# Kernel optimization log

Measured on AMD Instinct MI355X. Metric: run time of the kernel, lower is better.

## Reference

```python
import jax, jax.numpy as jnp
import numpy as np

B, S, H, U = 32, 2048, 1024, 1024


def setup_inputs() -> dict:
    key = jax.random.key(0)
    ks = jax.random.split(key, 8)
    sH = 1.0 / np.sqrt(H)
    sU = 1.0 / np.sqrt(U)
    return {
        "encoder_output": jax.random.normal(ks[0], (B, S, H), dtype=jnp.float32),
        "last_layer_h_n": jax.random.normal(ks[1], (B, H), dtype=jnp.float32),
        # torch Linear stores weight [out,in]; we store transposed [in,out] for x @ W
        "W1_w": jax.random.uniform(ks[2], (H, U), jnp.float32, -sH, sH),
        "W1_b": jax.random.uniform(ks[3], (U,), jnp.float32, -sH, sH),
        "W2_w": jax.random.uniform(ks[4], (H, U), jnp.float32, -sH, sH),
        "W2_b": jax.random.uniform(ks[5], (U,), jnp.float32, -sH, sH),
        "V_w": jax.random.uniform(ks[6], (U, 1), jnp.float32, -sU, sU),
        "V_b": jax.random.uniform(ks[7], (1,), jnp.float32, -sU, sU),
    }


def reference(encoder_output, last_layer_h_n, W1_w, W1_b, W2_w, W2_b, V_w, V_b):
    # proj_enc: [B,S,U]; proj_h: [B,1,U] (unsqueeze(1) broadcast)
    proj_enc = jnp.einsum("bsh,hu->bsu", encoder_output, W1_w) + W1_b
    proj_h = (last_layer_h_n @ W2_w + W2_b)[:, None, :]
    # score: [B,S,1]
    score = jnp.tanh(proj_enc + proj_h) @ V_w + V_b
    # softmax over the sequence axis (dim 1)
    attention_weights = jax.nn.softmax(score, axis=1)
    # NOTE: in the original module context_vector is always None (dead branch),
    # so the faithful output is attention_weights alone.
    return attention_weights
```

## Files before the change

### kernel.cpp

```cpp
#include <hip/hip_runtime.h>
#include <hip/hip_bf16.h>


typedef __bf16 bf16x8 __attribute__((ext_vector_type(8)));
typedef float  f32x4  __attribute__((ext_vector_type(4)));

#define HDIM 1024
#define UDIM 1024
#define SDIM 2048
#define MROWS 65536
#define BM 128
#define BN 128
#define BK 32

__device__ inline unsigned short f2bf(float x) {
    return __builtin_bit_cast(unsigned short, (__bf16)x);
}

__device__ inline float fast_tanh(float x) {
    float z = __expf(-2.0f * __builtin_fabsf(x));
    float t = __fdividef(1.0f - z, 1.0f + z);
    return __builtin_copysignf(t, x);
}

#define GLDS16(gp, lp)                                                              \
    __builtin_amdgcn_global_load_lds(                                               \
        (const __attribute__((address_space(1))) unsigned int*)(gp),                \
        (__attribute__((address_space(3))) unsigned int*)(lp), 16, 0, 0)

__global__ __launch_bounds__(256) void cvt_kernel(const float* __restrict__ in,
                                                  unsigned short* __restrict__ out) {
    size_t i = ((size_t)blockIdx.x * 256 + threadIdx.x) * 8;
    const float4 f0 = *(const float4*)(in + i);
    const float4 f1 = *(const float4*)(in + i + 4);
    ushort4 h0, h1;
    h0.x = f2bf(f0.x); h0.y = f2bf(f0.y); h0.z = f2bf(f0.z); h0.w = f2bf(f0.w);
    h1.x = f2bf(f1.x); h1.y = f2bf(f1.y); h1.z = f2bf(f1.z); h1.w = f2bf(f1.w);
    *(ushort4*)(out + i) = h0;
    *(ushort4*)(out + i + 4) = h1;
}

__global__ void w1t_kernel(const float* __restrict__ W1, unsigned short* __restrict__ W1T) {
    __shared__ float tile[32][33];
    int bx = blockIdx.x;
    int by = blockIdx.y;
    int tx = threadIdx.x, ty = threadIdx.y;
#pragma unroll
    for (int r = 0; r < 4; ++r) {
        int h = by * 32 + ty + r * 8;
        int u = bx * 32 + tx;
        tile[ty + r * 8][tx] = W1[h * UDIM + u];
    }
    __syncthreads();
#pragma unroll
    for (int r = 0; r < 4; ++r) {
        int u = bx * 32 + ty + r * 8;
        int h = by * 32 + tx;
        W1T[u * HDIM + h] = f2bf(tile[tx][ty + r * 8]);
    }
}

__global__ void php_kernel(const float* __restrict__ hn, const float* __restrict__ W2,
                           float* __restrict__ php) {
    int u = (blockIdx.x & 3) * 256 + threadIdx.x;
    int b = blockIdx.y;
    int hc = blockIdx.z;
    int h0 = hc * 128;
    float acc = 0.f;
#pragma unroll 8
    for (int h = h0; h < h0 + 128; ++h)
        acc = fmaf(hn[b * HDIM + h], W2[h * UDIM + u], acc);
    php[(hc * 32 + b) * UDIM + u] = acc;
}

__global__ void ph_combine(const float* __restrict__ php, const float* __restrict__ W1b,
                           const float* __restrict__ W2b, float* __restrict__ ph) {
    int idx = blockIdx.x * 256 + threadIdx.x;
    int u = idx & (UDIM - 1);
    int b = idx >> 10;
    float acc = W1b[u] + W2b[u];
#pragma unroll
    for (int p = 0; p < 8; ++p) acc += php[(p * 32 + b) * UDIM + u];
    ph[idx] = acc;
}

__global__ __launch_bounds__(256) void score_kernel(
    const unsigned short* __restrict__ encb, const unsigned short* __restrict__ W1T,
    const float* __restrict__ ph, const float* __restrict__ Vw,
    float* __restrict__ part) {
    __shared__ unsigned short As[BM * BK];
    __shared__ unsigned short Bs[BN * BK];

    const int bx = blockIdx.x;
    const int x = bx & 7;
    const int k = bx >> 3;
    const int tile_n = k & 7;
    const int tile_m = (x << 6) | (k >> 3);

    const int t = threadIdx.x;
    const int lane = t & 63;
    const int wid = t >> 6;
    const int wm = wid >> 1, wn = wid & 1;

    const int row0 = tile_m * BM;
    const int col0 = tile_n * BN;

    f32x4 acc[4][4];
#pragma unroll
    for (int i = 0; i < 4; ++i)
#pragma unroll
        for (int j = 0; j < 4; ++j)
            acc[i][j] = (f32x4){0.f, 0.f, 0.f, 0.f};

    const int mrow = lane & 15;
    const int kcs = ((lane >> 4) ^ ((mrow >> 1) & 3)) * 8;

    const int c0 = wid * 64 + lane;
    const int c1 = c0 + 256;
    const int r0c = c0 >> 2, r1c = c1 >> 2;
    const int kl0 = ((c0 & 3) ^ ((c0 >> 3) & 3)) * 8;
    const int kl1 = ((c1 & 3) ^ ((c1 >> 3) & 3)) * 8;
    const unsigned ldsA0 = (unsigned)(wid * 64) * 16;
    const unsigned ldsA1 = ldsA0 + 256 * 16;

    for (int kt = 0; kt < HDIM; kt += BK) {
        {
            const unsigned short* ga0 = encb + (size_t)(row0 + r0c) * HDIM + kt + kl0;
            const unsigned short* ga1 = encb + (size_t)(row0 + r1c) * HDIM + kt + kl1;
            const unsigned short* gb0 = W1T + (size_t)(col0 + r0c) * HDIM + kt + kl0;
            const unsigned short* gb1 = W1T + (size_t)(col0 + r1c) * HDIM + kt + kl1;
            GLDS16(ga0, (char*)As + ldsA0);
            GLDS16(ga1, (char*)As + ldsA1);
            GLDS16(gb0, (char*)Bs + ldsA0);
            GLDS16(gb1, (char*)Bs + ldsA1);
        }
        __syncthreads();

        bf16x8 a[4], bb[4];
#pragma unroll
        for (int i = 0; i < 4; ++i)
            a[i] = *reinterpret_cast<const bf16x8*>(As + (wm * 64 + i * 16 + mrow) * BK + kcs);
#pragma unroll
        for (int j = 0; j < 4; ++j)
            bb[j] = *reinterpret_cast<const bf16x8*>(Bs + (wn * 64 + j * 16 + mrow) * BK + kcs);
#pragma unroll
        for (int i = 0; i < 4; ++i)
#pragma unroll
            for (int j = 0; j < 4; ++j)
                acc[i][j] = __builtin_amdgcn_mfma_f32_16x16x32_bf16(a[i], bb[j], acc[i][j], 0, 0, 0);
        __syncthreads();
    }

    const int b = row0 >> 11;
    const int colg = lane & 15;
    const int rowq = (lane >> 4) * 4;
    float vw[4], phv[4];
#pragma unroll
    for (int j = 0; j < 4; ++j) {
        int u = col0 + wn * 64 + j * 16 + colg;
        vw[j] = Vw[u];
        phv[j] = ph[b * UDIM + u];
    }
#pragma unroll
    for (int i = 0; i < 4; ++i) {
#pragma unroll
        for (int r = 0; r < 4; ++r) {
            float s = 0.f;
#pragma unroll
            for (int j = 0; j < 4; ++j) {
                float pe = acc[i][j][r] + phv[j];
                s += fast_tanh(pe) * vw[j];
            }
            s += __shfl_xor(s, 1);
            s += __shfl_xor(s, 2);
            s += __shfl_xor(s, 4);
            s += __shfl_xor(s, 8);
            if (colg == 0) {
                int row = row0 + wm * 64 + i * 16 + rowq + r;
                part[(size_t)(tile_n * 2 + wn) * MROWS + row] = s;
            }
        }
    }
}

#define LDK 40
__global__ __launch_bounds__(256) void score_kernel_f32(
    const float* __restrict__ enc, const unsigned short* __restrict__ W1T,
    const float* __restrict__ ph, const float* __restrict__ Vw,
    float* __restrict__ part) {
    __shared__ unsigned short As[BM * LDK];
    __shared__ unsigned short Bs[BN * LDK];

    const int bx = blockIdx.x;
    const int tile_n = bx & 7;
    const int tile_m = bx >> 3;
    const int t = threadIdx.x;
    const int lane = t & 63;
    const int wid = t >> 6;
    const int wm = wid >> 1, wn = wid & 1;

    const int row0 = tile_m * BM;
    const int col0 = tile_n * BN;

    f32x4 acc[4][4];
#pragma unroll
    for (int i = 0; i < 4; ++i)
#pragma unroll
        for (int j = 0; j < 4; ++j)
            acc[i][j] = (f32x4){0.f, 0.f, 0.f, 0.f};

    const int mrow = lane & 15;
    const int kq = (lane >> 4) * 8;

    for (int kt = 0; kt < HDIM; kt += BK) {
        __syncthreads();
#pragma unroll
        for (int i = 0; i < 4; ++i) {
            int c = t + 256 * i;
            int r = c >> 3;
            int kc = (c & 7) * 4;
            const float4 f = *(const float4*)(enc + (size_t)(row0 + r) * HDIM + kt + kc);
            ushort4 h;
            h.x = f2bf(f.x); h.y = f2bf(f.y); h.z = f2bf(f.z); h.w = f2bf(f.w);
            *(ushort4*)(As + r * LDK + kc) = h;
        }
#pragma unroll
        for (int i = 0; i < 2; ++i) {
            int c = t + 256 * i;
            int r = c >> 2;
            int kc = (c & 3) * 8;
            const uint4 v = *(const uint4*)(W1T + (size_t)(col0 + r) * HDIM + kt + kc);
            *(uint4*)(Bs + r * LDK + kc) = v;
        }
        __syncthreads();

        bf16x8 a[4], bb[4];
#pragma unroll
        for (int i = 0; i < 4; ++i)
            a[i] = *reinterpret_cast<const bf16x8*>(As + (wm * 64 + i * 16 + mrow) * LDK + kq);
#pragma unroll
        for (int j = 0; j < 4; ++j)
            bb[j] = *reinterpret_cast<const bf16x8*>(Bs + (wn * 64 + j * 16 + mrow) * LDK + kq);
#pragma unroll
        for (int i = 0; i < 4; ++i)
#pragma unroll
            for (int j = 0; j < 4; ++j)
                acc[i][j] = __builtin_amdgcn_mfma_f32_16x16x32_bf16(a[i], bb[j], acc[i][j], 0, 0, 0);
    }

    const int b = row0 >> 11;
    const int colg = lane & 15;
    const int rowq = (lane >> 4) * 4;
    float vw[4], phv[4];
#pragma unroll
    for (int j = 0; j < 4; ++j) {
        int u = col0 + wn * 64 + j * 16 + colg;
        vw[j] = Vw[u];
        phv[j] = ph[b * UDIM + u];
    }
#pragma unroll
    for (int i = 0; i < 4; ++i) {
#pragma unroll
        for (int r = 0; r < 4; ++r) {
            float s = 0.f;
#pragma unroll
            for (int j = 0; j < 4; ++j) {
                float pe = acc[i][j][r] + phv[j];
                s += fast_tanh(pe) * vw[j];
            }
            s += __shfl_xor(s, 1);
            s += __shfl_xor(s, 2);
            s += __shfl_xor(s, 4);
            s += __shfl_xor(s, 8);
            if (colg == 0) {
                int row = row0 + wm * 64 + i * 16 + rowq + r;
                part[(size_t)(tile_n * 2 + wn) * MROWS + row] = s;
            }
        }
    }
}

__global__ void softmax_kernel(const float* __restrict__ part, float* __restrict__ out) {
    int b = blockIdx.x;
    int t = threadIdx.x;
    __shared__ float sred[4];
    float v[8];
    float lmax = -3.4e38f;
#pragma unroll
    for (int i = 0; i < 8; ++i) {
        int s = t + i * 256;
        float sum = 0.f;
#pragma unroll
        for (int p = 0; p < 16; ++p) sum += part[(size_t)p * MROWS + b * SDIM + s];
        v[i] = sum;
        lmax = fmaxf(lmax, sum);
    }
#pragma unroll
    for (int off = 1; off < 64; off <<= 1) lmax = fmaxf(lmax, __shfl_xor(lmax, off));
    if ((t & 63) == 0) sred[t >> 6] = lmax;
    __syncthreads();
    float bmax = fmaxf(fmaxf(sred[0], sred[1]), fmaxf(sred[2], sred[3]));
    __syncthreads();
    float lsum = 0.f;
#pragma unroll
    for (int i = 0; i < 8; ++i) {
        v[i] = expf(v[i] - bmax);
        lsum += v[i];
    }
#pragma unroll
    for (int off = 1; off < 64; off <<= 1) lsum += __shfl_xor(lsum, off);
    if ((t & 63) == 0) sred[t >> 6] = lsum;
    __syncthreads();
    float inv = 1.0f / (sred[0] + sred[1] + sred[2] + sred[3]);
#pragma unroll
    for (int i = 0; i < 8; ++i) out[b * SDIM + t + i * 256] = v[i] * inv;
}

extern "C" void kernel_launch(void* const* d_in, const int* in_sizes, int n_in,
                              void* d_out, int out_size, void* d_ws, size_t ws_size,
                              hipStream_t stream) {
    const float* enc = (const float*)d_in[0];
    const float* hn  = (const float*)d_in[1];
    const float* W1  = (const float*)d_in[2];
    const float* W1b = (const float*)d_in[3];
    const float* W2  = (const float*)d_in[4];
    const float* W2b = (const float*)d_in[5];
    const float* Vw  = (const float*)d_in[6];
    float* out = (float*)d_out;

    char* ws = (char*)d_ws;
    const size_t ENCB_BYTES = (size_t)MROWS * HDIM * 2;
    const size_t NEED = ENCB_BYTES + (2u << 20) + (128u << 10) + (1u << 20) + (4u << 20);

    if (ws_size >= NEED) {
        unsigned short* encb = (unsigned short*)ws;
        unsigned short* W1T  = (unsigned short*)(ws + ENCB_BYTES);
        float* ph   = (float*)(ws + ENCB_BYTES + (2u << 20));
        float* php  = (float*)(ws + ENCB_BYTES + (2u << 20) + (128u << 10));
        float* part = (float*)(ws + ENCB_BYTES + (2u << 20) + (128u << 10) + (1u << 20));

        cvt_kernel<<<32768, 256, 0, stream>>>(enc, encb);
        w1t_kernel<<<dim3(32, 32), dim3(32, 8), 0, stream>>>(W1, W1T);
        php_kernel<<<dim3(4, 32, 8), 256, 0, stream>>>(hn, W2, php);
        ph_combine<<<128, 256, 0, stream>>>(php, W1b, W2b, ph);
        score_kernel<<<dim3(4096), 256, 0, stream>>>(encb, W1T, ph, Vw, part);
        softmax_kernel<<<32, 256, 0, stream>>>(part, out);
    } else {
        unsigned short* W1T = (unsigned short*)ws;
        float* ph   = (float*)(ws + (2u << 20));
        float* php  = (float*)(ws + (2u << 20) + (128u << 10));
        float* part = (float*)(ws + (2u << 20) + (128u << 10) + (1u << 20));

        w1t_kernel<<<dim3(32, 32), dim3(32, 8), 0, stream>>>(W1, W1T);
        php_kernel<<<dim3(4, 32, 8), 256, 0, stream>>>(hn, W2, php);
        ph_combine<<<128, 256, 0, stream>>>(php, W1b, W2b, ph);
        score_kernel_f32<<<dim3(4096), 256, 0, stream>>>(enc, W1T, ph, Vw, part);
        softmax_kernel<<<32, 256, 0, stream>>>(part, out);
    }
}
```

Baseline: 591.8 us.

## Replace score GEMM with 256x256 double-buffered 8-wave pipelined kernel

The bf16 score GEMM moves from 128x128 tiles with BK=32 and a single LDS buffer to 256x256 tiles with BK=64, 512 threads and a 128KB double-buffered LDS ring. Global-to-LDS loads for the next stages are interleaved with MFMA phases under raw barriers and setprio. Per-wave partial scores are reduced in LDS before writing, so only 4 partials per row remain and a matching softmax kernel sums 4 instead of 16. The larger tile is meant to raise arithmetic intensity and hide load latency, at the cost of fragile manual vmcnt/barrier scheduling and one block per CU because of LDS use.

```diff
diff --git a/kernel.cpp b/kernel.cpp
--- a/kernel.cpp
+++ b/kernel.cpp
@@ -9,9 +9,7 @@
 #define UDIM 1024
 #define SDIM 2048
 #define MROWS 65536
-#define BM 128
-#define BN 128
-#define BK 32
+#define NT 16
 
 __device__ inline unsigned short f2bf(float x) {
     return __builtin_bit_cast(unsigned short, (__bf16)x);
@@ -84,19 +82,193 @@
     ph[idx] = acc;
 }
 
-__global__ __launch_bounds__(256) void score_kernel(
+__global__ __launch_bounds__(512, 2) void score_kernel2(
     const unsigned short* __restrict__ encb, const unsigned short* __restrict__ W1T,
     const float* __restrict__ ph, const float* __restrict__ Vw,
     float* __restrict__ part) {
-    __shared__ unsigned short As[BM * BK];
-    __shared__ unsigned short Bs[BN * BK];
+    __shared__ __align__(16) unsigned short smem[65536];
 
     const int bx = blockIdx.x;
     const int x = bx & 7;
     const int k = bx >> 3;
-    const int tile_n = k & 7;
-    const int tile_m = (x << 6) | (k >> 3);
-
+    const int tile_n = k & 3;
+    const int tile_m = (x << 5) | (k >> 2);
+    const int row0 = tile_m * 256;
+    const int col0 = tile_n * 256;
+
+    const int t = threadIdx.x;
+    const int lane = t & 63;
+    const int wid = t >> 6;
+    const int wm = wid >> 2;
+    const int wn = wid & 3;
+
+    const int e = lane & 7;
+    const int c = lane >> 4;
+    const int swz16 = (((c ^ (e & 3)) | ((e >> 2) << 2)) << 4);
+    const int offk0 = ((lane & 15) << 7) + swz16;
+    const int bhalf_off = (wn & 1) * 8192;
+
+    const int rp0 = (wid << 3) + (lane >> 3);
+    const int gsw = ((lane & 7) ^ (rp0 & 7)) << 3;
+    const size_t gof0 = (size_t)rp0 * HDIM + gsw;
+    const size_t gof1 = gof0 + (size_t)64 * HDIM;
+    const unsigned lof0 = (unsigned)(wid << 10);
+    const unsigned lof1 = lof0 + 8192u;
+
+    const unsigned short* gA0 = encb + (size_t)row0 * HDIM;
+    const unsigned short* gA1 = encb + (size_t)(row0 + 128) * HDIM;
+    const unsigned short* gB0 = W1T + (size_t)col0 * HDIM;
+    const unsigned short* gB1 = W1T + (size_t)(col0 + 128) * HDIM;
+
+#define STAGE(gbase, kt, slotbyte)                                          \
+    do {                                                                    \
+        GLDS16((gbase) + (kt) + gof0, (char*)smem + (slotbyte) + lof0);     \
+        GLDS16((gbase) + (kt) + gof1, (char*)smem + (slotbyte) + lof1);     \
+    } while (0)
+
+#define LOADA(half)                                                                          \
+    _Pragma("unroll") for (int fi = 0; fi < 4; ++fi)                                         \
+    _Pragma("unroll") for (int ks = 0; ks < 2; ++ks)                                         \
+        aF[fi][ks] = *(const bf16x8*)((const char*)smem + slotA + ((half) + fi) * 2048 +     \
+                                      (offk0 ^ (ks << 6)));
+
+#define LOADB(dst, jhalf)                                                                    \
+    _Pragma("unroll") for (int fj = 0; fj < 2; ++fj)                                         \
+    _Pragma("unroll") for (int ks = 0; ks < 2; ++ks)                                         \
+        dst[fj][ks] = *(const bf16x8*)((const char*)smem + slotB + bhalf_off +               \
+                                       ((jhalf) + fj) * 2048 + (offk0 ^ (ks << 6)));
+
+#define MFMA8(iBase, jBase, AF, BF)                                                          \
+    _Pragma("unroll") for (int fi = 0; fi < 4; ++fi)                                         \
+    _Pragma("unroll") for (int fj = 0; fj < 2; ++fj)                                         \
+    _Pragma("unroll") for (int ks = 0; ks < 2; ++ks)                                         \
+        acc[(iBase) + fi][(jBase) + fj] = __builtin_amdgcn_mfma_f32_16x16x32_bf16(           \
+            AF[fi][ks], BF[fj][ks], acc[(iBase) + fi][(jBase) + fj], 0, 0, 0);
+
+#define SBAR __builtin_amdgcn_s_barrier()
+
+    f32x4 acc[8][4];
+#pragma unroll
+    for (int i = 0; i < 8; ++i)
+#pragma unroll
+        for (int j = 0; j < 4; ++j)
+            acc[i][j] = (f32x4){0.f, 0.f, 0.f, 0.f};
+
+    STAGE(gB0, 0, 0u);
+    STAGE(gA0, 0, 16384u);
+    STAGE(gA1, 0, 32768u);
+    STAGE(gB1, 0, 49152u);
+    STAGE(gB0, 64, 65536u);
+    STAGE(gA0, 64, 81920u);
+    asm volatile("s_waitcnt vmcnt(4)" ::: "memory");
+    SBAR;
+
+#pragma unroll 2
+    for (int tau = 0; tau < NT; ++tau) {
+        const unsigned sbase = (tau & 1) ? 65536u : 0u;
+        const unsigned obase = 65536u - sbase;
+        const unsigned slotA = sbase + (unsigned)(1 + wm) * 16384u;
+        const unsigned slotB = sbase + ((wn & 2) ? 49152u : 0u);
+        const int ktn1 = (tau + 1) * 64;
+        const int ktn2 = (tau + 2) * 64;
+
+        bf16x8 aF[4][2], bJ0[2][2], bJ1[2][2];
+
+        LOADA(0);
+        LOADB(bJ0, 0);
+        if (tau + 1 < NT) STAGE(gA1, ktn1, obase + 32768u);
+        SBAR;
+        __builtin_amdgcn_s_setprio(1);
+        MFMA8(0, 0, aF, bJ0);
+        __builtin_amdgcn_s_setprio(0);
+        SBAR;
+
+        LOADB(bJ1, 2);
+        if (tau + 1 < NT) STAGE(gB1, ktn1, obase + 49152u);
+        SBAR;
+        __builtin_amdgcn_s_setprio(1);
+        MFMA8(0, 2, aF, bJ1);
+        __builtin_amdgcn_s_setprio(0);
+        SBAR;
+
+        LOADA(4);
+        if (tau + 2 < NT) STAGE(gB0, ktn2, sbase + 0u);
+        SBAR;
+        __builtin_amdgcn_s_setprio(1);
+        MFMA8(4, 2, aF, bJ1);
+        __builtin_amdgcn_s_setprio(0);
+        SBAR;
+
+        if (tau + 2 < NT) STAGE(gA0, ktn2, sbase + 16384u);
+        SBAR;
+        __builtin_amdgcn_s_setprio(1);
+        MFMA8(4, 0, aF, bJ0);
+        __builtin_amdgcn_s_setprio(0);
+        if (tau < NT - 1) {
+            if (tau == NT - 2) { asm volatile("s_waitcnt vmcnt(0)" ::: "memory"); }
+            else               { asm volatile("s_waitcnt vmcnt(4)" ::: "memory"); }
+            SBAR;
+        }
+    }
+
+    __syncthreads();
+    const int bidx = row0 >> 11;
+    const int colg = lane & 15;
+    const int rowq = (lane >> 4) << 2;
+    float vw[4], phv[4];
+#pragma unroll
+    for (int j = 0; j < 4; ++j) {
+        int u = col0 + wn * 64 + j * 16 + colg;
+        vw[j] = Vw[u];
+        phv[j] = ph[bidx * UDIM + u];
+    }
+    float* red = (float*)smem;
+#pragma unroll
+    for (int i = 0; i < 8; ++i) {
+#pragma unroll
+        for (int r = 0; r < 4; ++r) {
+            float s = 0.f;
+#pragma unroll
+            for (int j = 0; j < 4; ++j) {
+                float pe = acc[i][j][r] + phv[j];
+                s += fast_tanh(pe) * vw[j];
+            }
+            s += __shfl_xor(s, 1);
+            s += __shfl_xor(s, 2);
+            s += __shfl_xor(s, 4);
+            s += __shfl_xor(s, 8);
+            if (colg == 0) red[wid * 128 + i * 16 + rowq + r] = s;
+        }
+    }
+    __syncthreads();
+    if (t < 256) {
+        int wmr = t >> 7;
+        int rl = t & 127;
+        float s = red[(wmr * 4 + 0) * 128 + rl] + red[(wmr * 4 + 1) * 128 + rl] +
+                  red[(wmr * 4 + 2) * 128 + rl] + red[(wmr * 4 + 3) * 128 + rl];
+        part[(size_t)tile_n * MROWS + row0 + t] = s;
+    }
+#undef STAGE
+#undef LOADA
+#undef LOADB
+#undef MFMA8
+#undef SBAR
+}
+
+#define BM 128
+#define BN 128
+#define BK 32
+#define LDK 40
+__global__ __launch_bounds__(256) void score_kernel_f32(
+    const float* __restrict__ enc, const unsigned short* __restrict__ W1T,
+    const float* __restrict__ ph, const float* __restrict__ Vw,
+    float* __restrict__ part) {
+    __shared__ unsigned short As[BM * LDK];
+    __shared__ unsigned short Bs[BN * LDK];
+
+    const int bx = blockIdx.x;
+    const int tile_n = bx & 7;
+    const int tile_m = bx >> 3;
     const int t = threadIdx.x;
     const int lane = t & 63;
     const int wid = t >> 6;
@@ -113,42 +285,42 @@
             acc[i][j] = (f32x4){0.f, 0.f, 0.f, 0.f};
 
     const int mrow = lane & 15;
-    const int kcs = ((lane >> 4) ^ ((mrow >> 1) & 3)) * 8;
-
-    const int c0 = wid * 64 + lane;
-    const int c1 = c0 + 256;
-    const int r0c = c0 >> 2, r1c = c1 >> 2;
-    const int kl0 = ((c0 & 3) ^ ((c0 >> 3) & 3)) * 8;
-    const int kl1 = ((c1 & 3) ^ ((c1 >> 3) & 3)) * 8;
-    const unsigned ldsA0 = (unsigned)(wid * 64) * 16;
-    const unsigned ldsA1 = ldsA0 + 256 * 16;
+    const int kq = (lane >> 4) * 8;
 
     for (int kt = 0; kt < HDIM; kt += BK) {
-        {
-            const unsigned short* ga0 = encb + (size_t)(row0 + r0c) * HDIM + kt + kl0;
-            const unsigned short* ga1 = encb + (size_t)(row0 + r1c) * HDIM + kt + kl1;
-            const unsigned short* gb0 = W1T + (size_t)(col0 + r0c) * HDIM + kt + kl0;
-            const unsigned short* gb1 = W1T + (size_t)(col0 + r1c) * HDIM + kt + kl1;
-            GLDS16(ga0, (char*)As + ldsA0);
-            GLDS16(ga1, (char*)As + ldsA1);
-            GLDS16(gb0, (char*)Bs + ldsA0);
-            GLDS16(gb1, (char*)Bs + ldsA1);
+        __syncthreads();
+#pragma unroll
+        for (int i = 0; i < 4; ++i) {
+            int cc = t + 256 * i;
+            int r = cc >> 3;
+            int kc = (cc & 7) * 4;
+            const float4 f = *(const float4*)(enc + (size_t)(row0 + r) * HDIM + kt + kc);
+            ushort4 h;
+            h.x = f2bf(f.x); h.y = f2bf(f.y); h.z = f2bf(f.z); h.w = f2bf(f.w);
+            *(ushort4*)(As + r * LDK + kc) = h;
+        }
+#pragma unroll
+        for (int i = 0; i < 2; ++i) {
+            int cc = t + 256 * i;
+            int r = cc >> 2;
+            int kc = (cc & 3) * 8;
+            const uint4 v = *(const uint4*)(W1T + (size_t)(col0 + r) * HDIM + kt + kc);
+            *(uint4*)(Bs + r * LDK + kc) = v;
         }
         __syncthreads();
 
         bf16x8 a[4], bb[4];
 #pragma unroll
         for (int i = 0; i < 4; ++i)
-            a[i] = *reinterpret_cast<const bf16x8*>(As + (wm * 64 + i * 16 + mrow) * BK + kcs);
+            a[i] = *reinterpret_cast<const bf16x8*>(As + (wm * 64 + i * 16 + mrow) * LDK + kq);
 #pragma unroll
         for (int j = 0; j < 4; ++j)
-            bb[j] = *reinterpret_cast<const bf16x8*>(Bs + (wn * 64 + j * 16 + mrow) * BK + kcs);
+            bb[j] = *reinterpret_cast<const bf16x8*>(Bs + (wn * 64 + j * 16 + mrow) * LDK + kq);
 #pragma unroll
         for (int i = 0; i < 4; ++i)
 #pragma unroll
             for (int j = 0; j < 4; ++j)
                 acc[i][j] = __builtin_amdgcn_mfma_f32_16x16x32_bf16(a[i], bb[j], acc[i][j], 0, 0, 0);
-        __syncthreads();
     }
 
     const int b = row0 >> 11;
@@ -183,104 +355,43 @@
     }
 }
 
-#define LDK 40
-__global__ __launch_bounds__(256) void score_kernel_f32(
-    const float* __restrict__ enc, const unsigned short* __restrict__ W1T,
-    const float* __restrict__ ph, const float* __restrict__ Vw,
-    float* __restrict__ part) {
-    __shared__ unsigned short As[BM * LDK];
-    __shared__ unsigned short Bs[BN * LDK];
-
-    const int bx = blockIdx.x;
-    const int tile_n = bx & 7;
-    const int tile_m = bx >> 3;
-    const int t = threadIdx.x;
-    const int lane = t & 63;
-    const int wid = t >> 6;
-    const int wm = wid >> 1, wn = wid & 1;
-
-    const int row0 = tile_m * BM;
-    const int col0 = tile_n * BN;
-
-    f32x4 acc[4][4];
-#pragma unroll
-    for (int i = 0; i < 4; ++i)
-#pragma unroll
-        for (int j = 0; j < 4; ++j)
-            acc[i][j] = (f32x4){0.f, 0.f, 0.f, 0.f};
-
-    const int mrow = lane & 15;
-    const int kq = (lane >> 4) * 8;
-
-    for (int kt = 0; kt < HDIM; kt += BK) {
-        __syncthreads();
-#pragma unroll
-        for (int i = 0; i < 4; ++i) {
-            int c = t + 256 * i;
-            int r = c >> 3;
-            int kc = (c & 7) * 4;
-            const float4 f = *(const float4*)(enc + (size_t)(row0 + r) * HDIM + kt + kc);
-            ushort4 h;
-            h.x = f2bf(f.x); h.y = f2bf(f.y); h.z = f2bf(f.z); h.w = f2bf(f.w);
-            *(ushort4*)(As + r * LDK + kc) = h;
-        }
-#pragma unroll
-        for (int i = 0; i < 2; ++i) {
-            int c = t + 256 * i;
-            int r = c >> 2;
-            int kc = (c & 3) * 8;
-            const uint4 v = *(const uint4*)(W1T + (size_t)(col0 + r) * HDIM + kt + kc);
-            *(uint4*)(Bs + r * LDK + kc) = v;
-        }
-        __syncthreads();
-
-        bf16x8 a[4], bb[4];
-#pragma unroll
-        for (int i = 0; i < 4; ++i)
-            a[i] = *reinterpret_cast<const bf16x8*>(As + (wm * 64 + i * 16 + mrow) * LDK + kq);
-#pragma unroll
-        for (int j = 0; j < 4; ++j)
-            bb[j] = *reinterpret_cast<const bf16x8*>(Bs + (wn * 64 + j * 16 + mrow) * LDK + kq);
-#pragma unroll
-        for (int i = 0; i < 4; ++i)
-#pragma unroll
-            for (int j = 0; j < 4; ++j)
-                acc[i][j] = __builtin_amdgcn_mfma_f32_16x16x32_bf16(a[i], bb[j], acc[i][j], 0, 0, 0);
-    }
-
-    const int b = row0 >> 11;
-    const int colg = lane & 15;
-    const int rowq = (lane >> 4) * 4;
-    float vw[4], phv[4];
-#pragma unroll
-    for (int j = 0; j < 4; ++j) {
-        int u = col0 + wn * 64 + j * 16 + colg;
-        vw[j] = Vw[u];
-        phv[j] = ph[b * UDIM + u];
-    }
-#pragma unroll
-    for (int i = 0; i < 4; ++i) {
-#pragma unroll
-        for (int r = 0; r < 4; ++r) {
-            float s = 0.f;
-#pragma unroll
-            for (int j = 0; j < 4; ++j) {
-                float pe = acc[i][j][r] + phv[j];
-                s += fast_tanh(pe) * vw[j];
-            }
-            s += __shfl_xor(s, 1);
-            s += __shfl_xor(s, 2);
-            s += __shfl_xor(s, 4);
-            s += __shfl_xor(s, 8);
-            if (colg == 0) {
-                int row = row0 + wm * 64 + i * 16 + rowq + r;
-                part[(size_t)(tile_n * 2 + wn) * MROWS + row] = s;
-            }
-        }
-    }
-}
-
-__global__ void softmax_kernel(const float* __restrict__ part, float* __restrict__ out) {
+__global__ void softmax4_kernel(const float* __restrict__ part, float* __restrict__ out) {
+    int b = blockIdx.x;
+    int t = threadIdx.x;
+    __shared__ float sred[4];
+    float v[8];
+    float lmax = -3.4e38f;
+#pragma unroll
+    for (int i = 0; i < 8; ++i) {
+        int s = t + i * 256;
+        float sum = 0.f;
+#pragma unroll
+        for (int p = 0; p < 4; ++p) sum += part[(size_t)p * MROWS + b * SDIM + s];
+        v[i] = sum;
+        lmax = fmaxf(lmax, sum);
+    }
+#pragma unroll
+    for (int off = 1; off < 64; off <<= 1) lmax = fmaxf(lmax, __shfl_xor(lmax, off));
+    if ((t & 63) == 0) sred[t >> 6] = lmax;
+    __syncthreads();
+    float bmax = fmaxf(fmaxf(sred[0], sred[1]), fmaxf(sred[2], sred[3]));
+    __syncthreads();
+    float lsum = 0.f;
+#pragma unroll
+    for (int i = 0; i < 8; ++i) {
+        v[i] = expf(v[i] - bmax);
+        lsum += v[i];
+    }
+#pragma unroll
+    for (int off = 1; off < 64; off <<= 1) lsum += __shfl_xor(lsum, off);
+    if ((t & 63) == 0) sred[t >> 6] = lsum;
+    __syncthreads();
+    float inv = 1.0f / (sred[0] + sred[1] + sred[2] + sred[3]);
+#pragma unroll
+    for (int i = 0; i < 8; ++i) out[b * SDIM + t + i * 256] = v[i] * inv;
+}
+
+__global__ void softmax16_kernel(const float* __restrict__ part, float* __restrict__ out) {
     int b = blockIdx.x;
     int t = threadIdx.x;
     __shared__ float sred[4];
@@ -343,8 +454,8 @@
         w1t_kernel<<<dim3(32, 32), dim3(32, 8), 0, stream>>>(W1, W1T);
         php_kernel<<<dim3(4, 32, 8), 256, 0, stream>>>(hn, W2, php);
         ph_combine<<<128, 256, 0, stream>>>(php, W1b, W2b, ph);
-        score_kernel<<<dim3(4096), 256, 0, stream>>>(encb, W1T, ph, Vw, part);
-        softmax_kernel<<<32, 256, 0, stream>>>(part, out);
+        score_kernel2<<<dim3(1024), 512, 0, stream>>>(encb, W1T, ph, Vw, part);
+        softmax4_kernel<<<32, 256, 0, stream>>>(part, out);
     } else {
         unsigned short* W1T = (unsigned short*)ws;
         float* ph   = (float*)(ws + (2u << 20));
@@ -355,6 +466,6 @@
         php_kernel<<<dim3(4, 32, 8), 256, 0, stream>>>(hn, W2, php);
         ph_combine<<<128, 256, 0, stream>>>(php, W1b, W2b, ph);
         score_kernel_f32<<<dim3(4096), 256, 0, stream>>>(enc, W1T, ph, Vw, part);
-        softmax_kernel<<<32, 256, 0, stream>>>(part, out);
-    }
-}
+        softmax16_kernel<<<32, 256, 0, stream>>>(part, out);
+    }
+}
```

New measurement: 550.7 us. 7.0% less time.
